# Kernel tuning notes

Measured on AMD Instinct MI355X. Metric: run time of the kernel, lower is better.

The kernel has to match this reference:

```python
import jax, jax.numpy as jnp
import numpy as np
from jax import lax

B = 2048; T = 16; K = 12; G = T * B; NODES = G * (K + 1)
ENC = 64; GIN = 32; GHID = 64; GOUT = 32; EMB = 32; DEMB = 16
DYN = 32; DEC = 128; TOUT = 25; GRID = (13, 3); SCONV = 64; C31 = 16
SOC = ((GRID[0] - 4 + 1) // 2) * C31  # 80
TE = EMB * 3 + DEMB + GOUT            # 144


def _lstm(xs, Wih, Whh, bih, bhh):
    # xs: (T, N, in) seq-first, torch LSTM gate order i,f,g,o
    n = xs.shape[1]; H = Whh.shape[1]
    def step(carry, x):
        h, c = carry
        g = x @ Wih.T + h @ Whh.T + bih + bhh
        i, f, gg, o = jnp.split(g, 4, axis=-1)
        c = jax.nn.sigmoid(f) * c + jax.nn.sigmoid(i) * jnp.tanh(gg)
        h = jax.nn.sigmoid(o) * jnp.tanh(c)
        return (h, c), h
    z = jnp.zeros((n, H), xs.dtype)
    (h, _), hs = lax.scan(step, (z, z), xs)
    return hs, h


def _gat(x, src, dst, W, a_s, a_d, b, n):
    # PyG GATConv, heads=1, self-loops already in src/dst, leaky slope 0.2
    xw = x @ W.T
    e = jax.nn.leaky_relu((xw @ a_s)[src] + (xw @ a_d)[dst], 0.2)
    m = jax.ops.segment_max(e, dst, num_segments=n)
    ex = jnp.exp(e - m[dst])
    den = jax.ops.segment_sum(ex, dst, num_segments=n)
    alpha = ex / den[dst]
    return jax.ops.segment_sum(xw[src] * alpha[:, None], dst, num_segments=n) + b


def setup_inputs() -> dict:
    key = jax.random.key(0)
    ks = iter(jax.random.split(key, 80))
    f = lambda *s: jax.random.normal(next(ks), s, jnp.float32) * 0.05
    base = np.arange(G, dtype=np.int32) * (K + 1)          # ego node of each group
    nb = (base[:, None] + 1 + np.arange(K, dtype=np.int32)).reshape(-1)
    ego = np.repeat(base, K)
    edge_index = jnp.asarray(np.stack([np.concatenate([nb, ego]), np.concatenate([ego, nb])]))
    batch_gat = jnp.asarray(np.repeat(np.arange(G, dtype=np.int32), K + 1))
    m = np.zeros((B, GRID[1] * GRID[0], ENC), bool); m[:, :K, :] = True
    masks = jnp.asarray(m.reshape(B, GRID[1], GRID[0], ENC))
    return dict(
        data_figure_x=f(NODES, 4), edge_index=edge_index, batch_gat=batch_gat,
        hist=f(T, B, 2), hist_va=f(T, B, 2), hist_dis=f(T, B, 1), hist_lane=f(T, B, 2),
        nbrs=f(T, B * K, 2), nbrs_va=f(T, B * K, 2), nbrs_dis=f(T, B * K, 1), nbrs_lane=f(T, B * K, 2),
        masks=masks, lat_enc=f(B, 3), lon_enc=f(B, 2),
        ip_emb_W=f(GIN, 4), ip_emb_b=f(GIN),
        gat1_W=f(GHID, GIN), gat1_as=f(GHID), gat1_ad=f(GHID), gat1_b=f(GHID),
        gat2_W=f(GOUT, GHID), gat2_as=f(GOUT), gat2_ad=f(GOUT), gat2_b=f(GOUT),
        pos_W=f(EMB, 2), pos_b=f(EMB), va_W=f(EMB, 2), va_b=f(EMB),
        dis_W=f(DEMB, 1), dis_b=f(DEMB), lane_W=f(EMB, 2), lane_b=f(EMB),
        enc_Wih=f(4 * ENC, TE), enc_Whh=f(4 * ENC, ENC), enc_bih=f(4 * ENC), enc_bhh=f(4 * ENC),
        ta_Wih=f(4 * ENC, TE), ta_Whh=f(4 * ENC, ENC), ta_bih=f(4 * ENC), ta_bhh=f(4 * ENC),
        ta_TA_W=f(T, T * ENC), ta_TA_b=f(T),
        dyn_W=f(DYN, ENC), dyn_b=f(DYN),
        sconv_W=f(SCONV, ENC, 3, 3), sconv_b=f(SCONV),
        conv31_W=f(C31, SCONV, 3, 1), conv31_b=f(C31),
        dec_Wih=f(4 * DEC, 2 * SOC + DYN + 5), dec_Whh=f(4 * DEC, DEC), dec_bih=f(4 * DEC), dec_bhh=f(4 * DEC),
        op_W=f(5, DEC), op_b=f(5),
        oplat_W=f(3, 2 * SOC + DYN), oplat_b=f(3), oplon_W=f(2, 2 * SOC + DYN), oplon_b=f(2))


def reference(data_figure_x, edge_index, batch_gat, hist, hist_va, hist_dis, hist_lane,
              nbrs, nbrs_va, nbrs_dis, nbrs_lane, masks, lat_enc, lon_enc,
              ip_emb_W, ip_emb_b, gat1_W, gat1_as, gat1_ad, gat1_b,
              gat2_W, gat2_as, gat2_ad, gat2_b,
              pos_W, pos_b, va_W, va_b, dis_W, dis_b, lane_W, lane_b,
              enc_Wih, enc_Whh, enc_bih, enc_bhh,
              ta_Wih, ta_Whh, ta_bih, ta_bhh, ta_TA_W, ta_TA_b,
              dyn_W, dyn_b, sconv_W, sconv_b, conv31_W, conv31_b,
              dec_Wih, dec_Whh, dec_bih, dec_bhh, op_W, op_b,
              oplat_W, oplat_b, oplon_W, oplon_b):
    n = data_figure_x.shape[0]
    lrelu = lambda x: jax.nn.leaky_relu(x, 0.1)
    loop = jnp.arange(n, dtype=edge_index.dtype)
    src = jnp.concatenate([edge_index[0], loop])
    dst = jnp.concatenate([edge_index[1], loop])
    h = lrelu(data_figure_x @ ip_emb_W.T + ip_emb_b)
    h = lrelu(_gat(h, src, dst, gat1_W, gat1_as, gat1_ad, gat1_b, n))
    h = lrelu(_gat(h, src, dst, gat2_W, gat2_as, gat2_ad, gat2_b, n))
    # first node per group -> ego (hist), rest -> neighbors (batch_gat sorted)
    first_idx = jnp.searchsorted(batch_gat, jnp.arange(G, dtype=batch_gat.dtype))
    hist_gat = h[first_idx].reshape(T, B, GOUT)          # dropout = eval identity
    nbr_mask = jnp.ones(n, bool).at[first_idx].set(False)
    nbr_idx = jnp.where(nbr_mask, size=n - G)[0]
    nbrs_gat = h[nbr_idx].reshape(T, -1, GOUT)
    emb = lambda x, W, b: lrelu(x @ W.T + b)
    ch = jnp.concatenate([emb(hist, pos_W, pos_b), emb(hist_va, va_W, va_b),
                          emb(hist_dis, dis_W, dis_b), emb(hist_lane, lane_W, lane_b), hist_gat], -1)
    cn = jnp.concatenate([emb(nbrs, pos_W, pos_b), emb(nbrs_va, va_W, va_b),
                          emb(nbrs_dis, dis_W, dis_b), emb(nbrs_lane, lane_W, lane_b), nbrs_gat], -1)
    # TA_LSTM: temporal attention over per-step hidden states
    hs, _ = _lstm(ch, ta_Wih, ta_Whh, ta_bih, ta_bhh)     # (T, B, ENC)
    total = hs.transpose(1, 0, 2).reshape(B, T * ENC)
    beta = jax.nn.softmax(jax.nn.relu(total @ ta_TA_W.T + ta_TA_b), axis=-1)
    hist_enc = lrelu(jnp.einsum('tbh,bt->bh', hs, beta) @ dyn_W.T + dyn_b)
    _, nbrs_enc = _lstm(cn, enc_Wih, enc_Whh, enc_bih, enc_bhh)   # (B*K, ENC)
    # masked_scatter_: fill True positions row-major with flattened nbrs_enc
    mflat = masks.reshape(-1)
    sidx = jnp.clip(jnp.cumsum(mflat) - 1, 0)
    soc = jnp.where(mflat, nbrs_enc.reshape(-1)[sidx], 0.0).reshape(masks.shape).astype(jnp.float32)
    soc = soc.transpose(0, 3, 2, 1)                       # (B, ENC, 13, 3)
    dn = ('NCHW', 'OIHW', 'NCHW')
    soc = lrelu(lax.conv_general_dilated(soc, sconv_W, (1, 1), 'VALID', dimension_numbers=dn)
                + sconv_b[None, :, None, None])
    soc = lrelu(lax.conv_general_dilated(soc, conv31_W, (1, 1), 'VALID', dimension_numbers=dn)
                + conv31_b[None, :, None, None])          # (B, C31, 9, 1)
    pad = ((0, 0), (0, 0), (1, 1), (0, 0))
    mx = lax.reduce_window(soc, -jnp.inf, lax.max, (1, 1, 2, 1), (1, 1, 2, 1), pad).reshape(-1, SOC)
    av = (lax.reduce_window(soc, 0.0, lax.add, (1, 1, 2, 1), (1, 1, 2, 1), pad) / 2.0).reshape(-1, SOC)
    enc = jnp.concatenate([mx, av, hist_enc], 1)          # (B, 2*SOC+DYN)
    lat_pred = jax.nn.softmax(enc @ oplat_W.T + oplat_b, axis=1)
    lon_pred = jax.nn.softmax(enc @ oplon_W.T + oplon_b, axis=1)
    encd = jnp.concatenate([enc, lat_enc, lon_enc], 1)
    rep = jnp.broadcast_to(encd[None], (TOUT,) + encd.shape)
    hs2, _ = _lstm(rep, dec_Wih, dec_Whh, dec_bih, dec_bhh)
    fut = hs2 @ op_W.T + op_b                             # (TOUT, B, 5)
    out = jnp.concatenate([fut[..., 0:2], jnp.exp(fut[..., 2:4]), jnp.tanh(fut[..., 4:5])], -1)
    return out, lat_pred, lon_pred
```

## Files before the change

kernel.cpp:

```cpp
#include <hip/hip_runtime.h>
#include <hip/hip_bf16.h>
#include <cstddef>
#include <cstdint>
#include <math.h>

typedef __hip_bfloat16 bf16;
typedef _Float16 f16;
typedef _Float16 f16x8 __attribute__((ext_vector_type(8)));
typedef _Float16 f16x2 __attribute__((ext_vector_type(2)));
typedef float f32x4 __attribute__((ext_vector_type(4)));
#define MFMA16(a,b,c) __builtin_amdgcn_mfma_f32_16x16x32_f16(a,b,c,0,0,0)

#define DEV __device__ __forceinline__
DEV float bff(bf16 x){ return __bfloat162float(x); }
DEV bf16 fbf(float x){ return __float2bfloat16(x); }
DEV float lr01(float x){ return x>0.f? x : 0.1f*x; }
DEV float lr02(float x){ return x>0.f? x : 0.2f*x; }
DEV float frcp(float x){ return __builtin_amdgcn_rcpf(x); }
DEV float sigm(float x){ return frcp(1.f+__expf(-x)); }
DEV float tanhe(float x){ float a=fabsf(x); float e=__expf(-2.f*a); float t=(1.f-e)*frcp(1.f+e); return x<0.f? -t : t; }
DEV void stout(void* out, int isf, size_t i, float v){
  if (isf) ((float*)out)[i] = v; else ((bf16*)out)[i] = fbf(v);
}
DEV float bfu_lo(unsigned u){ return __uint_as_float(u << 16); }
DEV float bfu_hi(unsigned u){ return __uint_as_float(u & 0xffff0000u); }

#define NBATCH 2048
#define TSEQ 16
#define KNB 12
#define NGRP 32768
#define NNODES 425984
#define NBK 24576
#define NTOUT 25

__global__ __launch_bounds__(256) void detect_k(const uint32_t* __restrict__ x, int* __restrict__ flag) {
  __shared__ int cnt;
  if (threadIdx.x == 0) cnt = 0;
  __syncthreads();
  float v = __uint_as_float(x[threadIdx.x]);
  float a = fabsf(v);
  if (a > 1e-12f && a < 100.f) atomicAdd(&cnt, 1);
  __syncthreads();
  if (threadIdx.x == 0) *flag = (cnt >= 128) ? 1 : 0;
}

#define NCVT 55
struct CvtArgs {
  const void* src[NCVT];
  unsigned off[NCVT];
  unsigned cnt[NCVT];
};

__global__ __launch_bounds__(256) void cvt_k(CvtArgs a, float* __restrict__ dst,
                                             const int* __restrict__ flag, unsigned total) {
  const int isf = *flag;
  for (size_t e = (size_t)blockIdx.x*256 + threadIdx.x; e < total; e += (size_t)gridDim.x*256) {
    int lo = 0, hi = NCVT-1;
    while (lo < hi) { int mid = (lo+hi+1)>>1; if ((size_t)a.off[mid] <= e) lo = mid; else hi = mid-1; }
    unsigned r = (unsigned)(e - a.off[lo]);
    float v = isf ? ((const float*)a.src[lo])[r] : bff(((const bf16*)a.src[lo])[r]);
    dst[e] = v;
  }
}

__global__ __launch_bounds__(256) void prep_k(
    const float* __restrict__ scW, const float* __restrict__ c31W,
    const float* __restrict__ g1W, const float* __restrict__ g2W,
    const float* __restrict__ encWhh, const float* __restrict__ taWhh,
    const float* __restrict__ decWhh,
    f16* __restrict__ wp1t, f16* __restrict__ wp2t,
    float* __restrict__ w1t, float* __restrict__ w2t,
    f16* __restrict__ wench, f16* __restrict__ wtah, f16* __restrict__ wdech) {
  int idx = blockIdx.x*256 + threadIdx.x;
  if (idx < 12288) {
    int o = idx & 63; int k = idx >> 6; int kh = k >> 6; int i = k & 63;
    wp1t[idx] = (f16)scW[((size_t)(o*64+i)*3 + kh)*3];
  } else if (idx < 15360) {
    int e = idx - 12288;
    int o = e & 15; int k = e >> 4; int kh = k >> 6; int i = k & 63;
    wp2t[e] = (f16)c31W[(size_t)(o*64+i)*3 + kh];
  } else if (idx < 17408) {
    int e = idx - 15360; int k = e >> 6, f = e & 63;
    w1t[e] = g1W[f*32 + k];
  } else if (idx < 19456) {
    int e = idx - 17408; int k = e >> 5, f = e & 31;
    w2t[e] = g2W[f*64 + k];
  } else if (idx < 35840) {
    int e = idx - 19456;
    wench[e] = (f16)encWhh[e];
  } else if (idx < 52224) {
    int e = idx - 35840;
    wtah[e] = (f16)taWhh[e];
  } else if (idx < 117760) {
    int e = idx - 52224;
    wdech[e] = (f16)decWhh[e];
  }
}

__global__ __launch_bounds__(256) void gat_dense1_k(const float* __restrict__ x,
    const float* __restrict__ ipW, const float* __restrict__ ipb,
    const float* __restrict__ Wt, const float* __restrict__ as_, const float* __restrict__ ad_,
    bf16* __restrict__ out, float* __restrict__ esed) {
  __shared__ float As[64][33];
  __shared__ float Ws[32][64];
  __shared__ float xs[64][4];
  __shared__ float wipw[128];
  __shared__ float wipb[32];
  const int tid = threadIdx.x;
  const size_t bm = (size_t)blockIdx.x * 64;
  ((float*)xs)[tid] = x[bm*4 + tid];
  if (tid < 128) wipw[tid] = ipW[tid];
  else if (tid < 160) wipb[tid-128] = ipb[tid-128];
  #pragma unroll
  for (int i = 0; i < 8; i++) ((float*)Ws)[tid + 256*i] = Wt[tid + 256*i];
  __syncthreads();
  #pragma unroll
  for (int i = 0; i < 8; i++) {
    int e = tid + 256*i; int v = e >> 5, f = e & 31;
    float a = wipb[f];
    #pragma unroll
    for (int k = 0; k < 4; k++) a += xs[v][k]*wipw[f*4+k];
    As[v][f] = lr01(a);
  }
  __syncthreads();
  const int v = tid >> 2, f0 = (tid & 3) * 16;
  float acc[16];
  #pragma unroll
  for (int i = 0; i < 16; i++) acc[i] = 0.f;
  #pragma unroll 8
  for (int k = 0; k < 32; k++) {
    float a = As[v][k];
    const float4* wr = (const float4*)&Ws[k][f0];
    #pragma unroll
    for (int q = 0; q < 4; q++) {
      float4 w4 = wr[q];
      acc[4*q+0] += a*w4.x; acc[4*q+1] += a*w4.y; acc[4*q+2] += a*w4.z; acc[4*q+3] += a*w4.w;
    }
  }
  bf16* op = out + (bm+v)*64 + f0;
  #pragma unroll
  for (int i = 0; i < 16; i++) op[i] = fbf(acc[i]);
  float es = 0.f, ed = 0.f;
  #pragma unroll
  for (int i = 0; i < 16; i++) { es += acc[i]*as_[f0+i]; ed += acc[i]*ad_[f0+i]; }
  es += __shfl_xor(es, 1); es += __shfl_xor(es, 2);
  ed += __shfl_xor(ed, 1); ed += __shfl_xor(ed, 2);
  if ((tid & 3) == 0) { esed[(bm+v)*2] = es; esed[(bm+v)*2+1] = ed; }
}

__global__ __launch_bounds__(256) void gat_dense2_k(const bf16* __restrict__ in,
    const float* __restrict__ Wt, const float* __restrict__ as_, const float* __restrict__ ad_,
    bf16* __restrict__ out, float* __restrict__ esed) {
  __shared__ float As[64][65];
  __shared__ float Ws[64][32];
  const int tid = threadIdx.x;
  const size_t bm = (size_t)blockIdx.x * 64;
  #pragma unroll
  for (int i = 0; i < 16; i++) {
    int lin = tid + 256*i;
    As[lin>>6][lin&63] = bff(in[bm*64 + lin]);
    if (i < 8) ((float*)Ws)[tid + 256*i] = Wt[tid + 256*i];
  }
  __syncthreads();
  const int v = tid >> 2, f0 = (tid & 3) * 8;
  float acc[8];
  #pragma unroll
  for (int i = 0; i < 8; i++) acc[i] = 0.f;
  #pragma unroll 8
  for (int k = 0; k < 64; k++) {
    float a = As[v][k];
    const float4* wr = (const float4*)&Ws[k][f0];
    #pragma unroll
    for (int q = 0; q < 2; q++) {
      float4 w4 = wr[q];
      acc[4*q+0] += a*w4.x; acc[4*q+1] += a*w4.y; acc[4*q+2] += a*w4.z; acc[4*q+3] += a*w4.w;
    }
  }
  bf16* op = out + (bm+v)*32 + f0;
  #pragma unroll
  for (int i = 0; i < 8; i++) op[i] = fbf(acc[i]);
  float es = 0.f, ed = 0.f;
  #pragma unroll
  for (int i = 0; i < 8; i++) { es += acc[i]*as_[f0+i]; ed += acc[i]*ad_[f0+i]; }
  es += __shfl_xor(es, 1); es += __shfl_xor(es, 2);
  ed += __shfl_xor(ed, 1); ed += __shfl_xor(ed, 2);
  if ((tid & 3) == 0) { esed[(bm+v)*2] = es; esed[(bm+v)*2+1] = ed; }
}

__global__ __launch_bounds__(256) void alpha_k(const float* __restrict__ esed, float* __restrict__ alph) {
  int g = blockIdx.x*256 + threadIdx.x;
  size_t base = (size_t)g*13;
  float esv[13], edv[13];
  #pragma unroll
  for (int i = 0; i < 13; i++) { esv[i] = esed[(base+i)*2]; edv[i] = esed[(base+i)*2+1]; }
  float* o = alph + (size_t)g*40;
  float e[13]; float m = -1e30f;
  #pragma unroll
  for (int i = 0; i < 13; i++) { float z = lr02(esv[i] + edv[0]); e[i] = z; m = fmaxf(m, z); }
  float den = 0.f;
  #pragma unroll
  for (int i = 0; i < 13; i++) { e[i] = __expf(e[i]-m); den += e[i]; }
  float inv = 1.f/den;
  #pragma unroll
  for (int i = 0; i < 13; i++) o[i] = e[i]*inv;
  #pragma unroll
  for (int j = 1; j <= 12; j++) {
    float z0 = lr02(esv[0] + edv[j]);
    float z1 = lr02(esv[j] + edv[j]);
    float mm = fmaxf(z0, z1);
    float a0 = __expf(z0-mm), a1 = __expf(z1-mm);
    float s = 1.f/(a0+a1);
    o[13 + 2*(j-1)] = a0*s;
    o[14 + 2*(j-1)] = a1*s;
  }
}

template<int F>
__global__ __launch_bounds__(256) void agg_bf_k(const bf16* __restrict__ xw, const float* __restrict__ alph,
                                                const float* __restrict__ bias, bf16* __restrict__ out) {
  size_t idx = (size_t)blockIdx.x*256 + threadIdx.x;
  int f = (int)(idx % F);
  size_t vn = idx / F;
  int node = (int)(vn % 13);
  size_t g = vn / 13;
  size_t base = g*13;
  const float* al = alph + g*40;
  float acc = 0.f;
  if (node == 0) {
    #pragma unroll
    for (int i = 0; i < 13; i++) acc += al[i] * bff(xw[(base+i)*F + f]);
  } else {
    float a0 = al[13 + 2*(node-1)], a1 = al[14 + 2*(node-1)];
    acc = a0*bff(xw[base*F + f]) + a1*bff(xw[(base+node)*F + f]);
  }
  out[idx] = fbf(lr01(acc + bias[f]));
}

template<bool NBR>
__global__ __launch_bounds__(256) void gemm_embed_mfma_k(
    const float* __restrict__ p_in, const float* __restrict__ v_in,
    const float* __restrict__ di_in, const float* __restrict__ l_in,
    const bf16* __restrict__ h2,
    const float* __restrict__ posW, const float* __restrict__ posb,
    const float* __restrict__ vaW, const float* __restrict__ vab,
    const float* __restrict__ disW, const float* __restrict__ disb,
    const float* __restrict__ laneW, const float* __restrict__ laneb,
    const float* __restrict__ W, f16* __restrict__ C, int t0) {
  __shared__ __align__(16) f16 As[128][40];
  __shared__ __align__(16) f16 Bs[128][40];
  const int tid = threadIdx.x;
  const int bm = blockIdx.x * 128, bn = blockIdx.y * 128;
  const int bz = blockIdx.z;
  const int mm = tid & 127, par = tid >> 7;
  int t, n2;
  if (NBR) { t = t0 + bz; n2 = bm + mm; }
  else { int gm = bm + mm; t = gm >> 11; n2 = gm & 2047; }
  const int NROW = NBR ? NBK : NBATCH;
  size_t rn = (size_t)t*NROW + n2;
  const float px0 = p_in[rn*2], px1 = p_in[rn*2+1];
  const float vx0 = v_in[rn*2], vx1 = v_in[rn*2+1];
  const float dx  = di_in[rn];
  const float lx0 = l_in[rn*2], lx1 = l_in[rn*2+1];
  const int b = NBR ? (n2 / KNB) : n2;
  const int node_off = NBR ? (1 + n2 % KNB) : 0;
  const bf16* h2p = h2 + (((size_t)t*NBATCH + b)*13 + node_off)*32;
  const int wn = bn + mm;
  const int l = tid & 63, wv = tid >> 6;
  const int lr = l & 15, lq = l >> 4;
  f32x4 acc[2][8];
  #pragma unroll
  for (int rt = 0; rt < 2; rt++)
    #pragma unroll
    for (int ct = 0; ct < 8; ct++) acc[rt][ct] = (f32x4){0.f,0.f,0.f,0.f};
  for (int ks = 0; ks < 5; ks++) {
    const int k0 = ks*32;
    #pragma unroll
    for (int e = 0; e < 16; e++) {
      int kk = par + 2*e;
      int f = k0 + kk;
      float val;
      if (f < 32) {
        val = lr01(px0*posW[f*2] + px1*posW[f*2+1] + posb[f]);
      } else if (f < 64) {
        int ff = f-32;
        val = lr01(vx0*vaW[ff*2] + vx1*vaW[ff*2+1] + vab[ff]);
      } else if (f < 80) {
        int ff = f-64;
        val = lr01(dx*disW[ff] + disb[ff]);
      } else if (f < 112) {
        int ff = f-80;
        val = lr01(lx0*laneW[ff*2] + lx1*laneW[ff*2+1] + laneb[ff]);
      } else if (f < 144) {
        val = bff(h2p[f-112]);
      } else val = 0.f;
      As[mm][kk] = (f16)val;
      Bs[mm][kk] = (f < 144) ? (f16)W[(size_t)wn*144 + f] : (f16)0.f;
    }
    __syncthreads();
    f16x8 a0 = *(const f16x8*)&As[wv*32 + lr][lq*8];
    f16x8 a1 = *(const f16x8*)&As[wv*32 + 16 + lr][lq*8];
    #pragma unroll
    for (int ct = 0; ct < 8; ct++) {
      f16x8 bfr = *(const f16x8*)&Bs[ct*16 + lr][lq*8];
      acc[0][ct] = MFMA16(a0, bfr, acc[0][ct]);
      acc[1][ct] = MFMA16(a1, bfr, acc[1][ct]);
    }
    __syncthreads();
  }
  #pragma unroll
  for (int rt = 0; rt < 2; rt++)
    #pragma unroll
    for (int ct = 0; ct < 8; ct++)
      #pragma unroll
      for (int rg = 0; rg < 4; rg++) {
        int row = wv*32 + rt*16 + lq*4 + rg;
        int col = ct*16 + lr;
        size_t orow = NBR ? ((size_t)bz*NBK + bm + row) : (size_t)(bm + row);
        C[orow*256 + bn + col] = (f16)acc[rt][ct][rg];
      }
}

__global__ __launch_bounds__(512, 4) void enc_mega_k(
    const float* __restrict__ p_in, const float* __restrict__ v_in,
    const float* __restrict__ di_in, const float* __restrict__ l_in,
    const bf16* __restrict__ h2,
    const float* __restrict__ posW, const float* __restrict__ posb,
    const float* __restrict__ vaW, const float* __restrict__ vab,
    const float* __restrict__ disW, const float* __restrict__ disb,
    const float* __restrict__ laneW, const float* __restrict__ laneb,
    const float* __restrict__ Wih, const f16* __restrict__ Whh16,
    const float* __restrict__ bih, const float* __restrict__ bhh,
    float* __restrict__ hstate) {
  __shared__ __align__(16) f16 As_s[2][16][168];
  __shared__ __align__(16) f16 h_s[2][16][72];
  __shared__ float gates[16][258];
  const int tid = threadIdx.x;
  const int r0 = blockIdx.x * 16;
  const int l = tid & 63, w = tid >> 6;
  const int lr = l & 15, lq = l >> 4;
  const int cu0 = w*16 + lr;
  const int cu1 = 128 + cu0;
  f16x8 bxw[2][5];
  f16x8 bhw[2][2];
  float bv[2];
  #pragma unroll
  for (int s = 0; s < 2; s++) {
    const int cu = s ? cu1 : cu0;
    const float* wr = Wih + (size_t)cu*144;
    #pragma unroll
    for (int ks = 0; ks < 5; ks++) {
      f16x8 v;
      #pragma unroll
      for (int j = 0; j < 8; j++) {
        int k = ks*32 + lq*8 + j;
        v[j] = (k < 144) ? (f16)wr[k] : (f16)0.f;
      }
      bxw[s][ks] = v;
    }
    #pragma unroll
    for (int kt = 0; kt < 2; kt++)
      bhw[s][kt] = *(const f16x8*)&Whh16[(size_t)cu*64 + kt*32 + lq*8];
    bv[s] = bih[cu] + bhh[cu];
  }
  const int prow = tid & 15;
  const int pq = tid >> 4;
  const int n2 = r0 + prow;
  const int bb = n2 / KNB;
  const int noff = 1 + n2 - bb*KNB;
  float c0 = 0.f, c1 = 0.f;
  float La = 0.f, Lb = 0.f;
  uint4 HA = {0,0,0,0};
  for (int i = tid; i < 16*64; i += 512) h_s[0][i>>6][i&63] = (f16)0.f;

#define ENC_ISSUE(TP) do {                                                   \
    const size_t rnp = (size_t)(TP)*NBK + n2;                                \
    if (pq < 4)       { float2 p = *(const float2*)(p_in + rnp*2); La = p.x; Lb = p.y; } \
    else if (pq < 8)  { float2 p = *(const float2*)(v_in + rnp*2); La = p.x; Lb = p.y; } \
    else if (pq < 10) { La = di_in[rnp]; }                                   \
    else if (pq < 14) { float2 p = *(const float2*)(l_in + rnp*2); La = p.x; Lb = p.y; } \
    else if (pq < 18) { HA = *(const uint4*)(h2 + (((size_t)(TP)*NBATCH + bb)*13 + noff)*32 + (pq-14)*8); } \
  } while (0)

#define ENC_STAGE(BUF) do {                                                  \
    if (pq < 20) {                                                           \
      const int f0 = pq*8;                                                   \
      f16x8 v;                                                               \
      if (f0 < 32) {                                                         \
        _Pragma("unroll")                                                    \
        for (int j = 0; j < 8; j++)                                          \
          v[j] = (f16)lr01(La*posW[(f0+j)*2] + Lb*posW[(f0+j)*2+1] + posb[f0+j]); \
      } else if (f0 < 64) {                                                  \
        _Pragma("unroll")                                                    \
        for (int j = 0; j < 8; j++) {                                        \
          int ff = f0+j-32;                                                  \
          v[j] = (f16)lr01(La*vaW[ff*2] + Lb*vaW[ff*2+1] + vab[ff]);         \
        }                                                                    \
      } else if (f0 < 80) {                                                  \
        _Pragma("unroll")                                                    \
        for (int j = 0; j < 8; j++) {                                        \
          int ff = f0+j-64;                                                  \
          v[j] = (f16)lr01(La*disW[ff] + disb[ff]);                          \
        }                                                                    \
      } else if (f0 < 112) {                                                 \
        _Pragma("unroll")                                                    \
        for (int j = 0; j < 8; j++) {                                        \
          int ff = f0+j-80;                                                  \
          v[j] = (f16)lr01(La*laneW[ff*2] + Lb*laneW[ff*2+1] + laneb[ff]);   \
        }                                                                    \
      } else if (f0 < 144) {                                                 \
        v[0] = (f16)bfu_lo(HA.x); v[1] = (f16)bfu_hi(HA.x);                  \
        v[2] = (f16)bfu_lo(HA.y); v[3] = (f16)bfu_hi(HA.y);                  \
        v[4] = (f16)bfu_lo(HA.z); v[5] = (f16)bfu_hi(HA.z);                  \
        v[6] = (f16)bfu_lo(HA.w); v[7] = (f16)bfu_hi(HA.w);                  \
      } else {                                                               \
        _Pragma("unroll")                                                    \
        for (int j = 0; j < 8; j++) v[j] = (f16)0.f;                         \
      }                                                                      \
      *(f16x8*)&As_s[BUF][prow][f0] = v;                                     \
    }                                                                        \
  } while (0)

  ENC_ISSUE(0);
  ENC_STAGE(0);
  __syncthreads();
  int cur = 0;
  #pragma unroll 1
  for (int t = 0; t < TSEQ; t++) {
    const int tp = (t+1 < TSEQ) ? t+1 : t;
    ENC_ISSUE(tp);
    {
      f16x8 ae0 = *(const f16x8*)&As_s[cur][lr][lq*8];
      f16x8 ae1 = *(const f16x8*)&As_s[cur][lr][32 + lq*8];
      f16x8 ae2 = *(const f16x8*)&As_s[cur][lr][64 + lq*8];
      f16x8 ae3 = *(const f16x8*)&As_s[cur][lr][96 + lq*8];
      f16x8 ae4 = *(const f16x8*)&As_s[cur][lr][128 + lq*8];
      f16x8 ah0 = *(const f16x8*)&h_s[cur][lr][lq*8];
      f16x8 ah1 = *(const f16x8*)&h_s[cur][lr][32 + lq*8];
      #pragma unroll
      for (int s = 0; s < 2; s++) {
        f32x4 a = (f32x4){0.f,0.f,0.f,0.f};
        a = MFMA16(ae0, bxw[s][0], a);
        a = MFMA16(ae1, bxw[s][1], a);
        a = MFMA16(ae2, bxw[s][2], a);
        a = MFMA16(ae3, bxw[s][3], a);
        a = MFMA16(ae4, bxw[s][4], a);
        a = MFMA16(ah0, bhw[s][0], a);
        a = MFMA16(ah1, bhw[s][1], a);
        const int cu = s ? cu1 : cu0;
        #pragma unroll
        for (int q = 0; q < 4; q++)
          gates[lq*4 + q][cu] = a[q] + bv[s];
      }
    }
    __syncthreads();
    {
      const int u0 = pq*2;
      const float* gr = &gates[prow][0];
      float gi0 = gr[u0],       gi1 = gr[u0+1];
      float gf0 = gr[64+u0],    gf1 = gr[64+u0+1];
      float gg0 = gr[128+u0],   gg1 = gr[128+u0+1];
      float go0 = gr[192+u0],   go1 = gr[192+u0+1];
      float cv0 = sigm(gf0)*c0 + sigm(gi0)*tanhe(gg0);
      float cv1 = sigm(gf1)*c1 + sigm(gi1)*tanhe(gg1);
      c0 = cv0; c1 = cv1;
      f16x2 hv;
      hv[0] = (f16)(sigm(go0)*tanhe(cv0));
      hv[1] = (f16)(sigm(go1)*tanhe(cv1));
      *(f16x2*)&h_s[cur^1][prow][u0] = hv;
    }
    ENC_STAGE(cur^1);
    __syncthreads();
    cur ^= 1;
  }
#undef ENC_ISSUE
#undef ENC_STAGE
  for (int i = tid; i < 16*64; i += 512)
    hstate[(size_t)(r0 + (i>>6))*64 + (i&63)] = (float)h_s[cur][i>>6][i&63];
}

__global__ __launch_bounds__(256, 2) void gemm_bt(const bf16* __restrict__ A, const float* __restrict__ W,
                                                  float* __restrict__ C, int M, int N, int Kd) {
  __shared__ __align__(16) float As[8][132];
  __shared__ __align__(16) float Bs[8][132];
  const int tid = threadIdx.x;
  const int bm = blockIdx.x * 128, bn = blockIdx.y * 128;
  const int tx = tid & 15, ty = tid >> 4;
  float acc[8][8];
  #pragma unroll
  for (int i = 0; i < 8; i++)
    #pragma unroll
    for (int j = 0; j < 8; j++) acc[i][j] = 0.f;
  for (int k0 = 0; k0 < Kd; k0 += 8) {
    #pragma unroll
    for (int i = 0; i < 4; i++) {
      int lin = tid + 256*i;
      int kk = lin & 7, mm = lin >> 3;
      int gk = k0 + kk;
      As[kk][mm] = (gk < Kd) ? bff(A[(size_t)(bm+mm)*Kd + gk]) : 0.f;
      Bs[kk][mm] = (gk < Kd) ? W[(size_t)(bn+mm)*Kd + gk] : 0.f;
    }
    __syncthreads();
    #pragma unroll
    for (int kk = 0; kk < 8; kk++) {
      float4 a0 = *(const float4*)&As[kk][ty*4];
      float4 a1 = *(const float4*)&As[kk][64+ty*4];
      float4 b0 = *(const float4*)&Bs[kk][tx*4];
      float4 b1 = *(const float4*)&Bs[kk][64+tx*4];
      float av[8] = {a0.x,a0.y,a0.z,a0.w,a1.x,a1.y,a1.z,a1.w};
      float bv[8] = {b0.x,b0.y,b0.z,b0.w,b1.x,b1.y,b1.z,b1.w};
      #pragma unroll
      for (int i = 0; i < 8; i++)
        #pragma unroll
        for (int j = 0; j < 8; j++) acc[i][j] += av[i]*bv[j];
    }
    __syncthreads();
  }
  #pragma unroll
  for (int i = 0; i < 8; i++) {
    int m = bm + (i>>2)*64 + ty*4 + (i&3);
    #pragma unroll
    for (int jh = 0; jh < 2; jh++) {
      float4 v = make_float4(acc[i][jh*4+0], acc[i][jh*4+1], acc[i][jh*4+2], acc[i][jh*4+3]);
      *(float4*)&C[(size_t)m*N + bn + jh*64 + tx*4] = v;
    }
  }
}

template<bool HALL>
__global__ __launch_bounds__(256) void lstm64_mfma_k(const f16* __restrict__ XW, const f16* __restrict__ Whh16,
    const float* __restrict__ bih, const float* __restrict__ bhh,
    float* __restrict__ hstate, float* __restrict__ cstate, float* __restrict__ h_all,
    int t0, int nsteps, int nrows) {
  __shared__ __align__(16) f16 h_s[16][72];
  __shared__ __align__(16) float gates[16][260];
  const int tid = threadIdx.x;
  const int r0 = blockIdx.x * 16;
  const int l = tid & 63, wv = tid >> 6;
  const int lr = l & 15, lq = l >> 4;
  const int u = l, rg = wv;
  f16x8 bf[4][2];
  #pragma unroll
  for (int ct = 0; ct < 4; ct++)
    #pragma unroll
    for (int kt = 0; kt < 2; kt++)
      bf[ct][kt] = *(const f16x8*)&Whh16[(size_t)(wv*64 + ct*16 + lr)*64 + kt*32 + lq*8];
  float bj4[4];
  #pragma unroll
  for (int g = 0; g < 4; g++) bj4[g] = bih[g*64+u] + bhh[g*64+u];
  if (t0 == 0) {
    for (int i = tid; i < 16*64; i += 256) h_s[i>>6][i&63] = (f16)0.f;
  } else {
    for (int i = tid; i < 16*64; i += 256) h_s[i>>6][i&63] = (f16)hstate[(size_t)r0*64 + i];
  }
  float c[4];
  #pragma unroll
  for (int q = 0; q < 4; q++) c[q] = (t0 == 0) ? 0.f : cstate[((size_t)r0 + rg*4 + q)*64 + u];
  __syncthreads();
  for (int s = 0; s < nsteps; s++) {
    f16x8 a0 = *(const f16x8*)&h_s[lr][lq*8];
    f16x8 a1 = *(const f16x8*)&h_s[lr][32 + lq*8];
    f32x4 acc[4];
    #pragma unroll
    for (int ct = 0; ct < 4; ct++) {
      acc[ct] = (f32x4){0.f,0.f,0.f,0.f};
      acc[ct] = MFMA16(a0, bf[ct][0], acc[ct]);
      acc[ct] = MFMA16(a1, bf[ct][1], acc[ct]);
    }
    #pragma unroll
    for (int ct = 0; ct < 4; ct++)
      #pragma unroll
      for (int q2 = 0; q2 < 4; q2++)
        gates[lq*4 + q2][wv*64 + ct*16 + lr] = acc[ct][q2];
    __syncthreads();
    const f16* xwrow = XW + ((size_t)s*nrows + r0)*256;
    #pragma unroll
    for (int q = 0; q < 4; q++) {
      const int r = rg*4 + q;
      float gi = gates[r][u]     + bj4[0] + (float)xwrow[(size_t)r*256 + u];
      float gf = gates[r][64+u]  + bj4[1] + (float)xwrow[(size_t)r*256 + 64 + u];
      float gg = gates[r][128+u] + bj4[2] + (float)xwrow[(size_t)r*256 + 128 + u];
      float go = gates[r][192+u] + bj4[3] + (float)xwrow[(size_t)r*256 + 192 + u];
      float cv = sigm(gf)*c[q] + sigm(gi)*tanhe(gg);
      c[q] = cv;
      float hv = sigm(go)*tanhe(cv);
      h_s[r][u] = (f16)hv;
      if (HALL) h_all[((size_t)(t0+s)*nrows + r0 + r)*64 + u] = hv;
    }
    __syncthreads();
  }
  #pragma unroll
  for (int q = 0; q < 4; q++) {
    const int r = rg*4 + q;
    hstate[((size_t)r0 + r)*64 + u] = (float)h_s[r][u];
    cstate[((size_t)r0 + r)*64 + u] = c[q];
  }
}

__global__ __launch_bounds__(512) void lstm128_mfma_k(const float* __restrict__ XW,
    const f16* __restrict__ Whh16, const float* __restrict__ bih, const float* __restrict__ bhh,
    int steps, float* __restrict__ h_all) {
  __shared__ __align__(16) f16 h_s[2][16][136];
  const int tid = threadIdx.x;
  const int r0 = blockIdx.x * 16;
  const int l = tid & 63, wv = tid >> 6;
  const int lr = l & 15, lq = l >> 4;
  const int u = wv*16 + lr;
  f16x8 bf[4][4];
  #pragma unroll
  for (int g = 0; g < 4; g++)
    #pragma unroll
    for (int kt = 0; kt < 4; kt++)
      bf[g][kt] = *(const f16x8*)&Whh16[(size_t)(g*128 + u)*128 + kt*32 + lq*8];
  float xr[4][4];
  #pragma unroll
  for (int g = 0; g < 4; g++) {
    float bj = bih[g*128 + u] + bhh[g*128 + u];
    #pragma unroll
    for (int rg = 0; rg < 4; rg++)
      xr[g][rg] = XW[(size_t)(r0 + lq*4 + rg)*512 + g*128 + u] + bj;
  }
  for (int i = tid; i < 16*128; i += 512) h_s[0][i>>7][i&127] = (f16)0.f;
  float c[4] = {0.f,0.f,0.f,0.f};
  __syncthreads();
  int cur = 0;
  for (int t = 0; t < steps; t++) {
    f16x8 a0 = *(const f16x8*)&h_s[cur][lr][lq*8];
    f16x8 a1 = *(const f16x8*)&h_s[cur][lr][32 + lq*8];
    f16x8 a2 = *(const f16x8*)&h_s[cur][lr][64 + lq*8];
    f16x8 a3 = *(const f16x8*)&h_s[cur][lr][96 + lq*8];
    f32x4 acc[4];
    #pragma unroll
    for (int g = 0; g < 4; g++) {
      acc[g] = (f32x4){0.f,0.f,0.f,0.f};
      acc[g] = MFMA16(a0, bf[g][0], acc[g]);
      acc[g] = MFMA16(a1, bf[g][1], acc[g]);
      acc[g] = MFMA16(a2, bf[g][2], acc[g]);
      acc[g] = MFMA16(a3, bf[g][3], acc[g]);
    }
    #pragma unroll
    for (int rg = 0; rg < 4; rg++) {
      const int row = lq*4 + rg;
      float gi = acc[0][rg] + xr[0][rg];
      float gf = acc[1][rg] + xr[1][rg];
      float gg = acc[2][rg] + xr[2][rg];
      float go = acc[3][rg] + xr[3][rg];
      float cv = sigm(gf)*c[rg] + sigm(gi)*tanhe(gg);
      c[rg] = cv;
      float hv = sigm(go)*tanhe(cv);
      h_s[cur^1][row][u] = (f16)hv;
      h_all[((size_t)t*NBATCH + r0 + row)*128 + u] = hv;
    }
    __syncthreads();
    cur ^= 1;
  }
}

__global__ __launch_bounds__(256) void ta_scores_k(const float* __restrict__ hs, const float* __restrict__ W,
                                                   const float* __restrict__ bias, float* __restrict__ sc) {
  int idx = blockIdx.x*256 + threadIdx.x;
  int i = idx & 15; int b = idx >> 4;
  float acc = bias[i];
  for (int t = 0; t < 16; t++) {
    const float* hr = hs + ((size_t)t*NBATCH + b)*64;
    const float* wr = W + (size_t)i*1024 + t*64;
    #pragma unroll
    for (int h = 0; h < 64; h++) acc += hr[h]*wr[h];
  }
  sc[idx] = fmaxf(acc, 0.f);
}

__global__ __launch_bounds__(256) void ta_ctx_k(const float* __restrict__ hs, const float* __restrict__ sc,
    const float* __restrict__ dynW, const float* __restrict__ dynb, float* __restrict__ henc) {
  int idx = blockIdx.x*256 + threadIdx.x;
  int o = idx & 31; int b = idx >> 5;
  const float* s = sc + (size_t)b*16;
  float m = s[0];
  #pragma unroll
  for (int t = 1; t < 16; t++) m = fmaxf(m, s[t]);
  float e[16]; float den = 0.f;
  #pragma unroll
  for (int t = 0; t < 16; t++) { e[t] = __expf(s[t]-m); den += e[t]; }
  float inv = 1.f/den;
  float acc = dynb[o];
  for (int t = 0; t < 16; t++) {
    const float* hr = hs + ((size_t)t*NBATCH + b)*64;
    float inner = 0.f;
    #pragma unroll
    for (int h = 0; h < 64; h++) inner += hr[h]*dynW[(size_t)o*64 + h];
    acc += (e[t]*inv)*inner;
  }
  henc[idx] = lr01(acc);
}

__global__ __launch_bounds__(256) void fused_conv_k(const float* __restrict__ nenc,
    const f16* __restrict__ wp1t, const f16* __restrict__ wp2t,
    const float* __restrict__ scb, const float* __restrict__ c31b,
    const float* __restrict__ henc, const float* __restrict__ lat_enc, const float* __restrict__ lon_enc,
    float* __restrict__ e192, bf16* __restrict__ encd) {
  __shared__ f16 ws1[12288];
  __shared__ f16 ws2[3072];
  __shared__ float img[4][13][64];
  __shared__ float c1s[4][64][12];
  __shared__ float c2s[4][16][9];
  const int tid = threadIdx.x;
  const int l = tid & 63, wv = tid >> 6;
  const int b = blockIdx.x*4 + wv;
  #pragma unroll
  for (int it = 0; it < 24; it++) ((uint32_t*)ws1)[tid + 256*it] = ((const uint32_t*)wp1t)[tid + 256*it];
  #pragma unroll
  for (int it = 0; it < 6; it++) ((uint32_t*)ws2)[tid + 256*it] = ((const uint32_t*)wp2t)[tid + 256*it];
  #pragma unroll
  for (int it = 0; it < 13; it++)
    img[wv][it][l] = (it < 12) ? nenc[((size_t)b*12 + it)*64 + l] : 0.f;
  __syncthreads();
  {
    const int o = l;
    float acc[11];
    float bv = scb[o];
    #pragma unroll
    for (int h = 0; h < 11; h++) acc[h] = bv;
    for (int k = 0; k < 192; k++) {
      int kh = k >> 6, i = k & 63;
      float w = (float)ws1[k*64 + o];
      const float* ic = img[wv][kh];
      #pragma unroll
      for (int h = 0; h < 11; h++) acc[h] += ic[h*64 + i] * w;
    }
    #pragma unroll
    for (int h = 0; h < 11; h++) c1s[wv][o][h] = lr01(acc[h]);
  }
  __syncthreads();
  if (l < 48) {
    const int o2 = l / 3, jg = l - o2*3;
    float acc[3];
    float bv = c31b[o2];
    #pragma unroll
    for (int m = 0; m < 3; m++) acc[m] = bv;
    for (int k = 0; k < 192; k++) {
      int kh = k >> 6, i = k & 63;
      float w = (float)ws2[k*16 + o2];
      #pragma unroll
      for (int m = 0; m < 3; m++) acc[m] += c1s[wv][i][jg*3 + m + kh] * w;
    }
    #pragma unroll
    for (int m = 0; m < 3; m++) c2s[wv][o2][jg*3 + m] = lr01(acc[m]);
  }
  __syncthreads();
  for (int it = 0; it < 4; it++) {
    int k = l + it*64;
    if (k >= 197) break;
    float val;
    if (k < 192) {
      if (k < 160) {
        bool is_av = (k >= 80);
        int rel = is_av ? (k - 80) : k;
        int o = rel / 5, p = rel - o*5;
        const float* r = c2s[wv][o];
        float v2 = r[2*p];
        if (p == 0) val = is_av ? v2*0.5f : v2;
        else { float v1 = r[2*p-1]; val = is_av ? (v1+v2)*0.5f : fmaxf(v1, v2); }
      } else {
        val = henc[(size_t)b*32 + (k-160)];
      }
      e192[(size_t)b*192 + k] = val;
    } else if (k < 195) {
      val = lat_enc[(size_t)b*3 + (k-192)];
    } else {
      val = lon_enc[(size_t)b*2 + (k-195)];
    }
    encd[(size_t)b*197 + k] = fbf(val);
  }
}

__global__ __launch_bounds__(256) void latlon_k(const float* __restrict__ e192,
    const float* __restrict__ latW, const float* __restrict__ latb,
    const float* __restrict__ lonW, const float* __restrict__ lonb,
    void* __restrict__ out, const int* __restrict__ flag) {
  int b = blockIdx.x*256 + threadIdx.x;
  const int isf = *flag;
  const float* e = e192 + (size_t)b*192;
  float s[3];
  #pragma unroll
  for (int c2 = 0; c2 < 3; c2++) {
    float acc = latb[c2];
    for (int k = 0; k < 192; k++) acc += e[k]*latW[c2*192+k];
    s[c2] = acc;
  }
  float m = fmaxf(s[0], fmaxf(s[1], s[2]));
  float e0 = __expf(s[0]-m), e1 = __expf(s[1]-m), e2 = __expf(s[2]-m);
  float inv = 1.f/(e0+e1+e2);
  stout(out, isf, 256000 + (size_t)b*3 + 0, e0*inv);
  stout(out, isf, 256000 + (size_t)b*3 + 1, e1*inv);
  stout(out, isf, 256000 + (size_t)b*3 + 2, e2*inv);
  float q[2];
  #pragma unroll
  for (int c2 = 0; c2 < 2; c2++) {
    float acc = lonb[c2];
    for (int k = 0; k < 192; k++) acc += e[k]*lonW[c2*192+k];
    q[c2] = acc;
  }
  float m2 = fmaxf(q[0], q[1]);
  float f0 = __expf(q[0]-m2), f1 = __expf(q[1]-m2);
  float inv2 = 1.f/(f0+f1);
  stout(out, isf, 262144 + (size_t)b*2 + 0, f0*inv2);
  stout(out, isf, 262144 + (size_t)b*2 + 1, f1*inv2);
}

__global__ __launch_bounds__(256) void out_k(const float* __restrict__ hs2, const float* __restrict__ opW,
                                             const float* __restrict__ opb,
                                             void* __restrict__ out, const int* __restrict__ flag) {
  int idx = blockIdx.x*256 + threadIdx.x;
  const int isf = *flag;
  const float* h = hs2 + (size_t)idx*128;
  float f[5];
  #pragma unroll
  for (int c2 = 0; c2 < 5; c2++) {
    float acc = opb[c2];
    #pragma unroll
    for (int k = 0; k < 128; k++) acc += h[k]*opW[c2*128+k];
    f[c2] = acc;
  }
  stout(out, isf, (size_t)idx*5 + 0, f[0]);
  stout(out, isf, (size_t)idx*5 + 1, f[1]);
  stout(out, isf, (size_t)idx*5 + 2, __expf(f[2]));
  stout(out, isf, (size_t)idx*5 + 3, __expf(f[3]));
  stout(out, isf, (size_t)idx*5 + 4, tanhe(f[4]));
}

static const size_t OFF_H2   = 0;
static const size_t OFF_P    = 6815744;
static const size_t OFF_Q    = 20447232;
static const size_t OFF_ESED = 34078720;
static const size_t OFF_ALPH = 34930688;
static const size_t OFF_XWTA = 6815744;
static const size_t OFF_HSTA = 15204352;
static const size_t OFF_SCO  = 17301504;
static const size_t OFF_HS2  = 6815744;
static const size_t OFF_HST  = 23691264;
static const size_t OFF_CST  = 25264128;
static const size_t OFF_E192 = 28573696;
static const size_t OFF_ENCD = 28966912;
static const size_t OFF_XWD  = 29168640;
static const size_t OFF_HEN  = 35000000;
static const size_t OFF_CVT  = 36241408;
static const size_t OFF_WP1T = 41280000;
static const size_t OFF_WP2T = 41286144;
static const size_t OFF_W1T  = 41287680;
static const size_t OFF_W2T  = 41289728;
static const size_t OFF_WENC = 41291776;
static const size_t OFF_WTAH = 41299968;
static const size_t OFF_WDECH= 41308160;
static const size_t OFF_FLAG = 41400000;

extern "C" void kernel_launch(void* const* d_in, const int* in_sizes, int n_in,
                              void* d_out, int out_size, void* d_ws, size_t ws_size,
                              hipStream_t stream) {
  (void)in_sizes; (void)n_in; (void)out_size; (void)ws_size;
  float* ws = (float*)d_ws;
  int* flag = (int*)(ws + OFF_FLAG);

  static const int   cidx[NCVT] = {0,3,4,5,6,7,8,9,10,12,13,
    14,15,16,17,18,19,20,21,22,23,24,25,26,27,28,29,30,31,
    32,33,34,35,36,37,38,39,40,41,42,43,44,45,46,47,
    48,49,50,51,52,53,54,55,56,57};
  static const unsigned ccnt[NCVT] = {1703936,65536,65536,32768,65536,786432,786432,393216,786432,6144,4096,
    128,32,2048,64,64,64,2048,32,32,32,64,32,64,32,16,16,64,32,
    36864,16384,256,256,36864,16384,256,256,16384,16,2048,32,36864,64,3072,16,
    100864,65536,512,512,640,5,576,3,384,2};
  CvtArgs ca;
  unsigned total = 0;
  float* cp[58];
  for (int i = 0; i < NCVT; i++) {
    ca.src[i] = d_in[cidx[i]];
    ca.off[i] = total;
    ca.cnt[i] = ccnt[i];
    cp[cidx[i]] = ws + OFF_CVT + total;
    total += ccnt[i];
  }
  detect_k<<<1,256,0,stream>>>((const uint32_t*)d_in[0], flag);
  cvt_k<<<4096,256,0,stream>>>(ca, ws + OFF_CVT, flag, total);

  void* out = d_out;
  bf16*  h2    = (bf16*)(ws + OFF_H2);
  bf16*  h1    = (bf16*)(ws + OFF_P);
  bf16*  xw1   = (bf16*)(ws + OFF_Q);
  bf16*  xw2   = (bf16*)(ws + OFF_Q);
  float* esed  = ws + OFF_ESED;
  float* alph  = ws + OFF_ALPH;
  f16*   xwta  = (f16*)(ws + OFF_XWTA);
  float* hsta  = ws + OFF_HSTA;
  float* sco   = ws + OFF_SCO;
  float* henc  = ws + OFF_HEN;
  float* hst   = ws + OFF_HST;
  float* cst   = ws + OFF_CST;
  float* e192  = ws + OFF_E192;
  bf16*  encd  = (bf16*)(ws + OFF_ENCD);
  float* xwd   = ws + OFF_XWD;
  f16*   wp1t  = (f16*)(ws + OFF_WP1T);
  f16*   wp2t  = (f16*)(ws + OFF_WP2T);
  float* w1t   = ws + OFF_W1T;
  float* w2t   = ws + OFF_W2T;
  f16*   wench = (f16*)(ws + OFF_WENC);
  f16*   wtah  = (f16*)(ws + OFF_WTAH);
  f16*   wdech = (f16*)(ws + OFF_WDECH);
  float* hs2   = ws + OFF_HS2;

  prep_k<<<460,256,0,stream>>>(cp[44], cp[46], cp[16], cp[20], cp[33], cp[37], cp[49],
                               wp1t, wp2t, w1t, w2t, wench, wtah, wdech);

  gat_dense1_k<<<6656,256,0,stream>>>(cp[0], cp[14], cp[15], w1t, cp[17], cp[18], xw1, esed);
  alpha_k<<<128,256,0,stream>>>(esed, alph);
  agg_bf_k<64><<<106496,256,0,stream>>>(xw1, alph, cp[19], h1);
  gat_dense2_k<<<6656,256,0,stream>>>(h1, w2t, cp[21], cp[22], xw2, esed);
  alpha_k<<<128,256,0,stream>>>(esed, alph);
  agg_bf_k<32><<<53248,256,0,stream>>>(xw2, alph, cp[23], h2);

  gemm_embed_mfma_k<false><<<dim3(256,2,1),256,0,stream>>>(cp[3], cp[4], cp[5], cp[6], h2,
      cp[24],cp[25],cp[26],cp[27],cp[28],cp[29],cp[30],cp[31], cp[36], xwta, 0);
  lstm64_mfma_k<true><<<128,256,0,stream>>>(xwta, wtah, cp[38], cp[39], hst, cst, hsta, 0, TSEQ, NBATCH);
  ta_scores_k<<<128,256,0,stream>>>(hsta, cp[40], cp[41], sco);
  ta_ctx_k<<<256,256,0,stream>>>(hsta, sco, cp[42], cp[43], henc);

  enc_mega_k<<<1536,512,0,stream>>>(cp[7], cp[8], cp[9], cp[10], h2,
      cp[24],cp[25],cp[26],cp[27],cp[28],cp[29],cp[30],cp[31],
      cp[32], wench, cp[34], cp[35], hst);

  fused_conv_k<<<512,256,0,stream>>>(hst, wp1t, wp2t, cp[45], cp[47], henc, cp[12], cp[13], e192, encd);

  latlon_k<<<8,256,0,stream>>>(e192, cp[54], cp[55], cp[56], cp[57], out, flag);
  gemm_bt<<<dim3(16,4),256,0,stream>>>(encd, cp[48], xwd, NBATCH, 512, 197);
  lstm128_mfma_k<<<128,512,0,stream>>>(xwd, wdech, cp[50], cp[51], NTOUT, hs2);
  out_k<<<200,256,0,stream>>>(hs2, cp[52], cp[53], out, flag);
}
```

Measured before the change: 802.4 us.

## Run the trajectory-attention LSTM as extra blocks inside the encoder mega kernel

The standalone 64-unit LSTM kernel, launched with only 128 blocks, is folded into the encoder mega kernel as 128 additional leading blocks. The two independent recurrences now run concurrently in one launch instead of back to back. This removes one launch and the idle-GPU time of the small serial LSTM. Shared memory is unioned between the two roles. The LSTM blocks use 512-thread blocks with only four active waves, which wastes some slots, and the attention kernels now wait on the combined launch.

```diff
diff --git a/kernel.cpp b/kernel.cpp
--- a/kernel.cpp
+++ b/kernel.cpp
@@ -320,7 +320,7 @@
       }
 }
 
-__global__ __launch_bounds__(512, 4) void enc_mega_k(
+__global__ __launch_bounds__(512, 4) void enc_ta_mega_k(
     const float* __restrict__ p_in, const float* __restrict__ v_in,
     const float* __restrict__ di_in, const float* __restrict__ l_in,
     const bf16* __restrict__ h2,
@@ -330,14 +330,78 @@
     const float* __restrict__ laneW, const float* __restrict__ laneb,
     const float* __restrict__ Wih, const f16* __restrict__ Whh16,
     const float* __restrict__ bih, const float* __restrict__ bhh,
-    float* __restrict__ hstate) {
-  __shared__ __align__(16) f16 As_s[2][16][168];
-  __shared__ __align__(16) f16 h_s[2][16][72];
-  __shared__ float gates[16][258];
+    float* __restrict__ hstate,
+    const f16* __restrict__ XWta, const f16* __restrict__ Whh16ta,
+    const float* __restrict__ bihta, const float* __restrict__ bhhta,
+    float* __restrict__ h_all_ta) {
+  __shared__ __align__(16) union SMem {
+    struct { f16 As_s[2][16][168]; f16 h_s[2][16][72]; float gates[16][258]; } e;
+    struct { f16 h_s[16][72]; float gates[16][260]; } a;
+  } sm;
   const int tid = threadIdx.x;
-  const int r0 = blockIdx.x * 16;
-  const int l = tid & 63, w = tid >> 6;
+  const int l = tid & 63;
   const int lr = l & 15, lq = l >> 4;
+
+  if (blockIdx.x < 128) {
+    const int r0 = blockIdx.x * 16;
+    const int wv = tid >> 6;
+    const int u = l, rg = wv;
+    f16x8 bf[4][2];
+    if (wv < 4) {
+      #pragma unroll
+      for (int ct = 0; ct < 4; ct++)
+        #pragma unroll
+        for (int kt = 0; kt < 2; kt++)
+          bf[ct][kt] = *(const f16x8*)&Whh16ta[(size_t)(wv*64 + ct*16 + lr)*64 + kt*32 + lq*8];
+    }
+    float bj4[4];
+    #pragma unroll
+    for (int g = 0; g < 4; g++) bj4[g] = bihta[g*64+u] + bhhta[g*64+u];
+    for (int i = tid; i < 16*64; i += 512) sm.a.h_s[i>>6][i&63] = (f16)0.f;
+    float c[4] = {0.f,0.f,0.f,0.f};
+    __syncthreads();
+    #pragma unroll 1
+    for (int s = 0; s < TSEQ; s++) {
+      if (wv < 4) {
+        f16x8 a0 = *(const f16x8*)&sm.a.h_s[lr][lq*8];
+        f16x8 a1 = *(const f16x8*)&sm.a.h_s[lr][32 + lq*8];
+        f32x4 acc[4];
+        #pragma unroll
+        for (int ct = 0; ct < 4; ct++) {
+          acc[ct] = (f32x4){0.f,0.f,0.f,0.f};
+          acc[ct] = MFMA16(a0, bf[ct][0], acc[ct]);
+          acc[ct] = MFMA16(a1, bf[ct][1], acc[ct]);
+        }
+        #pragma unroll
+        for (int ct = 0; ct < 4; ct++)
+          #pragma unroll
+          for (int q2 = 0; q2 < 4; q2++)
+            sm.a.gates[lq*4 + q2][wv*64 + ct*16 + lr] = acc[ct][q2];
+      }
+      __syncthreads();
+      if (wv < 4) {
+        const f16* xwrow = XWta + ((size_t)s*NBATCH + r0)*256;
+        #pragma unroll
+        for (int q = 0; q < 4; q++) {
+          const int r = rg*4 + q;
+          float gi = sm.a.gates[r][u]     + bj4[0] + (float)xwrow[(size_t)r*256 + u];
+          float gf = sm.a.gates[r][64+u]  + bj4[1] + (float)xwrow[(size_t)r*256 + 64 + u];
+          float gg = sm.a.gates[r][128+u] + bj4[2] + (float)xwrow[(size_t)r*256 + 128 + u];
+          float go = sm.a.gates[r][192+u] + bj4[3] + (float)xwrow[(size_t)r*256 + 192 + u];
+          float cv = sigm(gf)*c[q] + sigm(gi)*tanhe(gg);
+          c[q] = cv;
+          float hv = sigm(go)*tanhe(cv);
+          sm.a.h_s[r][u] = (f16)hv;
+          h_all_ta[((size_t)s*NBATCH + r0 + r)*64 + u] = hv;
+        }
+      }
+      __syncthreads();
+    }
+    return;
+  }
+
+  const int r0 = (blockIdx.x - 128) * 16;
+  const int w = tid >> 6;
   const int cu0 = w*16 + lr;
   const int cu1 = 128 + cu0;
   f16x8 bxw[2][5];
@@ -370,7 +434,7 @@
   float c0 = 0.f, c1 = 0.f;
   float La = 0.f, Lb = 0.f;
   uint4 HA = {0,0,0,0};
-  for (int i = tid; i < 16*64; i += 512) h_s[0][i>>6][i&63] = (f16)0.f;
+  for (int i = tid; i < 16*64; i += 512) sm.e.h_s[0][i>>6][i&63] = (f16)0.f;
 
 #define ENC_ISSUE(TP) do {                                                   \
     const size_t rnp = (size_t)(TP)*NBK + n2;                                \
@@ -416,7 +480,7 @@
         _Pragma("unroll")                                                    \
         for (int j = 0; j < 8; j++) v[j] = (f16)0.f;                         \
       }                                                                      \
-      *(f16x8*)&As_s[BUF][prow][f0] = v;                                     \
+      *(f16x8*)&sm.e.As_s[BUF][prow][f0] = v;                                \
     }                                                                        \
   } while (0)
 
@@ -429,13 +493,13 @@
     const int tp = (t+1 < TSEQ) ? t+1 : t;
     ENC_ISSUE(tp);
     {
-      f16x8 ae0 = *(const f16x8*)&As_s[cur][lr][lq*8];
-      f16x8 ae1 = *(const f16x8*)&As_s[cur][lr][32 + lq*8];
-      f16x8 ae2 = *(const f16x8*)&As_s[cur][lr][64 + lq*8];
-      f16x8 ae3 = *(const f16x8*)&As_s[cur][lr][96 + lq*8];
-      f16x8 ae4 = *(const f16x8*)&As_s[cur][lr][128 + lq*8];
-      f16x8 ah0 = *(const f16x8*)&h_s[cur][lr][lq*8];
-      f16x8 ah1 = *(const f16x8*)&h_s[cur][lr][32 + lq*8];
+      f16x8 ae0 = *(const f16x8*)&sm.e.As_s[cur][lr][lq*8];
+      f16x8 ae1 = *(const f16x8*)&sm.e.As_s[cur][lr][32 + lq*8];
+      f16x8 ae2 = *(const f16x8*)&sm.e.As_s[cur][lr][64 + lq*8];
+      f16x8 ae3 = *(const f16x8*)&sm.e.As_s[cur][lr][96 + lq*8];
+      f16x8 ae4 = *(const f16x8*)&sm.e.As_s[cur][lr][128 + lq*8];
+      f16x8 ah0 = *(const f16x8*)&sm.e.h_s[cur][lr][lq*8];
+      f16x8 ah1 = *(const f16x8*)&sm.e.h_s[cur][lr][32 + lq*8];
       #pragma unroll
       for (int s = 0; s < 2; s++) {
         f32x4 a = (f32x4){0.f,0.f,0.f,0.f};
@@ -449,13 +513,13 @@
         const int cu = s ? cu1 : cu0;
         #pragma unroll
         for (int q = 0; q < 4; q++)
-          gates[lq*4 + q][cu] = a[q] + bv[s];
+          sm.e.gates[lq*4 + q][cu] = a[q] + bv[s];
       }
     }
     __syncthreads();
     {
       const int u0 = pq*2;
-      const float* gr = &gates[prow][0];
+      const float* gr = &sm.e.gates[prow][0];
       float gi0 = gr[u0],       gi1 = gr[u0+1];
       float gf0 = gr[64+u0],    gf1 = gr[64+u0+1];
       float gg0 = gr[128+u0],   gg1 = gr[128+u0+1];
@@ -466,7 +530,7 @@
       f16x2 hv;
       hv[0] = (f16)(sigm(go0)*tanhe(cv0));
       hv[1] = (f16)(sigm(go1)*tanhe(cv1));
-      *(f16x2*)&h_s[cur^1][prow][u0] = hv;
+      *(f16x2*)&sm.e.h_s[cur^1][prow][u0] = hv;
     }
     ENC_STAGE(cur^1);
     __syncthreads();
@@ -475,7 +539,7 @@
 #undef ENC_ISSUE
 #undef ENC_STAGE
   for (int i = tid; i < 16*64; i += 512)
-    hstate[(size_t)(r0 + (i>>6))*64 + (i&63)] = (float)h_s[cur][i>>6][i&63];
+    hstate[(size_t)(r0 + (i>>6))*64 + (i&63)] = (float)sm.e.h_s[cur][i>>6][i&63];
 }
 
 __global__ __launch_bounds__(256, 2) void gemm_bt(const bf16* __restrict__ A, const float* __restrict__ W,
@@ -523,76 +587,6 @@
       float4 v = make_float4(acc[i][jh*4+0], acc[i][jh*4+1], acc[i][jh*4+2], acc[i][jh*4+3]);
       *(float4*)&C[(size_t)m*N + bn + jh*64 + tx*4] = v;
     }
-  }
-}
-
-template<bool HALL>
-__global__ __launch_bounds__(256) void lstm64_mfma_k(const f16* __restrict__ XW, const f16* __restrict__ Whh16,
-    const float* __restrict__ bih, const float* __restrict__ bhh,
-    float* __restrict__ hstate, float* __restrict__ cstate, float* __restrict__ h_all,
-    int t0, int nsteps, int nrows) {
-  __shared__ __align__(16) f16 h_s[16][72];
-  __shared__ __align__(16) float gates[16][260];
-  const int tid = threadIdx.x;
-  const int r0 = blockIdx.x * 16;
-  const int l = tid & 63, wv = tid >> 6;
-  const int lr = l & 15, lq = l >> 4;
-  const int u = l, rg = wv;
-  f16x8 bf[4][2];
-  #pragma unroll
-  for (int ct = 0; ct < 4; ct++)
-    #pragma unroll
-    for (int kt = 0; kt < 2; kt++)
-      bf[ct][kt] = *(const f16x8*)&Whh16[(size_t)(wv*64 + ct*16 + lr)*64 + kt*32 + lq*8];
-  float bj4[4];
-  #pragma unroll
-  for (int g = 0; g < 4; g++) bj4[g] = bih[g*64+u] + bhh[g*64+u];
-  if (t0 == 0) {
-    for (int i = tid; i < 16*64; i += 256) h_s[i>>6][i&63] = (f16)0.f;
-  } else {
-    for (int i = tid; i < 16*64; i += 256) h_s[i>>6][i&63] = (f16)hstate[(size_t)r0*64 + i];
-  }
-  float c[4];
-  #pragma unroll
-  for (int q = 0; q < 4; q++) c[q] = (t0 == 0) ? 0.f : cstate[((size_t)r0 + rg*4 + q)*64 + u];
-  __syncthreads();
-  for (int s = 0; s < nsteps; s++) {
-    f16x8 a0 = *(const f16x8*)&h_s[lr][lq*8];
-    f16x8 a1 = *(const f16x8*)&h_s[lr][32 + lq*8];
-    f32x4 acc[4];
-    #pragma unroll
-    for (int ct = 0; ct < 4; ct++) {
-      acc[ct] = (f32x4){0.f,0.f,0.f,0.f};
-      acc[ct] = MFMA16(a0, bf[ct][0], acc[ct]);
-      acc[ct] = MFMA16(a1, bf[ct][1], acc[ct]);
-    }
-    #pragma unroll
-    for (int ct = 0; ct < 4; ct++)
-      #pragma unroll
-      for (int q2 = 0; q2 < 4; q2++)
-        gates[lq*4 + q2][wv*64 + ct*16 + lr] = acc[ct][q2];
-    __syncthreads();
-    const f16* xwrow = XW + ((size_t)s*nrows + r0)*256;
-    #pragma unroll
-    for (int q = 0; q < 4; q++) {
-      const int r = rg*4 + q;
-      float gi = gates[r][u]     + bj4[0] + (float)xwrow[(size_t)r*256 + u];
-      float gf = gates[r][64+u]  + bj4[1] + (float)xwrow[(size_t)r*256 + 64 + u];
-      float gg = gates[r][128+u] + bj4[2] + (float)xwrow[(size_t)r*256 + 128 + u];
-      float go = gates[r][192+u] + bj4[3] + (float)xwrow[(size_t)r*256 + 192 + u];
-      float cv = sigm(gf)*c[q] + sigm(gi)*tanhe(gg);
-      c[q] = cv;
-      float hv = sigm(go)*tanhe(cv);
-      h_s[r][u] = (f16)hv;
-      if (HALL) h_all[((size_t)(t0+s)*nrows + r0 + r)*64 + u] = hv;
-    }
-    __syncthreads();
-  }
-  #pragma unroll
-  for (int q = 0; q < 4; q++) {
-    const int r = rg*4 + q;
-    hstate[((size_t)r0 + r)*64 + u] = (float)h_s[r][u];
-    cstate[((size_t)r0 + r)*64 + u] = c[q];
   }
 }
 
@@ -892,7 +886,6 @@
   float* sco   = ws + OFF_SCO;
   float* henc  = ws + OFF_HEN;
   float* hst   = ws + OFF_HST;
-  float* cst   = ws + OFF_CST;
   float* e192  = ws + OFF_E192;
   bf16*  encd  = (bf16*)(ws + OFF_ENCD);
   float* xwd   = ws + OFF_XWD;
@@ -917,13 +910,14 @@
 
   gemm_embed_mfma_k<false><<<dim3(256,2,1),256,0,stream>>>(cp[3], cp[4], cp[5], cp[6], h2,
       cp[24],cp[25],cp[26],cp[27],cp[28],cp[29],cp[30],cp[31], cp[36], xwta, 0);
-  lstm64_mfma_k<true><<<128,256,0,stream>>>(xwta, wtah, cp[38], cp[39], hst, cst, hsta, 0, TSEQ, NBATCH);
+
+  enc_ta_mega_k<<<1664,512,0,stream>>>(cp[7], cp[8], cp[9], cp[10], h2,
+      cp[24],cp[25],cp[26],cp[27],cp[28],cp[29],cp[30],cp[31],
+      cp[32], wench, cp[34], cp[35], hst,
+      xwta, wtah, cp[38], cp[39], hsta);
+
   ta_scores_k<<<128,256,0,stream>>>(hsta, cp[40], cp[41], sco);
   ta_ctx_k<<<256,256,0,stream>>>(hsta, sco, cp[42], cp[43], henc);
-
-  enc_mega_k<<<1536,512,0,stream>>>(cp[7], cp[8], cp[9], cp[10], h2,
-      cp[24],cp[25],cp[26],cp[27],cp[28],cp[29],cp[30],cp[31],
-      cp[32], wench, cp[34], cp[35], hst);
 
   fused_conv_k<<<512,256,0,stream>>>(hst, wp1t, wp2t, cp[45], cp[47], henc, cp[12], cp[13], e192, encd);
 
```

Measured after the change: 788.5 us. No clear change (-1.7%).
